# Kernel optimization log

Measured on AMD Instinct MI355X. Metric: run time of the kernel, lower is better.

Reference implementation:

```python
import jax, jax.numpy as jnp
import numpy as np

E = 256  # embed_dim == input_chn (required by ln_ff broadcast)
B = 256
LAMBDA_INIT = float(0.8 - 0.6 * np.exp(-0.3 * 1.0))  # layer_index = 1


def rmsnorm(x, scale, d, eps=1e-8):
    # matches torch RMSNorm: rms = ||x||_2 / sqrt(d); x / (rms + eps) * scale
    norm = jnp.linalg.norm(x, axis=-1, keepdims=True)
    rms = norm * (d ** -0.5)
    return scale * (x / (rms + eps))


def setup_inputs() -> dict:
    key = jax.random.key(0)
    ks = jax.random.split(key, 12)
    x = jax.random.normal(ks[0], (B, E, E), jnp.float32)
    s = 0.02
    return {
        "x": x,
        "Wq": jax.random.normal(ks[1], (E, 2 * E), jnp.float32) * s,
        "bq": jnp.zeros((2 * E,), jnp.float32),
        "Wk": jax.random.normal(ks[2], (E, 2 * E), jnp.float32) * s,
        "bk": jnp.zeros((2 * E,), jnp.float32),
        "Wv": jax.random.normal(ks[3], (E, E), jnp.float32) * s,
        "bv": jnp.zeros((E,), jnp.float32),
        "lq1": jax.random.normal(ks[4], (E,), jnp.float32) * 0.1,
        "lk1": jax.random.normal(ks[5], (E,), jnp.float32) * 0.1,
        "lq2": jax.random.normal(ks[6], (E,), jnp.float32) * 0.1,
        "lk2": jax.random.normal(ks[7], (E,), jnp.float32) * 0.1,
        "ln_attn_scale": jnp.ones((E,), jnp.float32),
        "norm_scale": jnp.ones((E,), jnp.float32),
        "ln_ff_scale": jnp.ones((E,), jnp.float32),
        "W1": jax.random.normal(ks[8], (E, 4 * E), jnp.float32) * s,
        "b1": jnp.zeros((4 * E,), jnp.float32),
        "W2": jax.random.normal(ks[9], (4 * E, E), jnp.float32) * s,
        "b2": jnp.zeros((E,), jnp.float32),
    }


def reference(x, Wq, bq, Wk, bk, Wv, bv, lq1, lk1, lq2, lk2,
              ln_attn_scale, norm_scale, ln_ff_scale, W1, b1, W2, b2):
    scale = E ** -0.25
    # a = ln_attn(x^T)^T  (normalize over seq dim which equals E)
    a = jnp.swapaxes(rmsnorm(jnp.swapaxes(x, -1, -2), ln_attn_scale, E), -1, -2)
    # decompose: moving average kernel=5, stride=1, edge-replicate padding 2 on seq dim
    ap = jnp.pad(a, ((0, 0), (2, 2), (0, 0)), mode="edge")
    trend = (ap[:, 0:-4] + ap[:, 1:-3] + ap[:, 2:-2] + ap[:, 3:-1] + ap[:, 4:]) / 5.0
    seasonal = a - trend
    # Q from trend, K from seasonal, V from a; all projected along the seq(=E) dim
    q = jnp.swapaxes(trend, -1, -2) @ Wq + bq          # [B, C, 2E]
    q1, q2 = jnp.split(q, 2, axis=-1)
    k = jnp.swapaxes(seasonal, -1, -2) @ Wk + bk       # [B, C, 2E]
    k1, k2 = jnp.split(k, 2, axis=-1)
    v = jnp.swapaxes(a, -1, -2) @ Wv + bv              # [B, C, E]
    a1 = jnp.einsum("bce,bde->bcd", q1, k1) * scale    # [B, C, C]
    a2 = jnp.einsum("bce,bde->bcd", q2, k2) * scale
    lam = jnp.exp(jnp.sum(lq1 * lk1)) - jnp.exp(jnp.sum(lq2 * lk2)) + LAMBDA_INIT
    d = jax.nn.softmax(a1, axis=-1) - lam * jax.nn.softmax(a2, axis=-1)
    attn = rmsnorm(d @ v, norm_scale, E) * (1.0 - LAMBDA_INIT)  # [B, C, E]
    x = x + jnp.swapaxes(attn, -1, -2)
    # FFN branch: ln_ff over last dim (chn == E), then project along seq dim
    h = jnp.swapaxes(rmsnorm(x, ln_ff_scale, E), -1, -2)        # [B, C, E]
    h = jax.nn.silu(h @ W1 + b1) @ W2 + b2                      # [B, C, E]
    x = x + jnp.swapaxes(h, -1, -2)
    return x
```

## Files before the change

kernel.cpp:

```cpp
#include <hip/hip_runtime.h>
#include <math.h>

static constexpr int E = 256;
static constexpr int BTOT = 256;

typedef __bf16 bf16;
typedef __bf16 bf16x8 __attribute__((ext_vector_type(8)));
typedef __bf16 bf16x4 __attribute__((ext_vector_type(4)));
typedef float f32x4 __attribute__((ext_vector_type(4)));

__device__ __forceinline__ void gload16(const void* g, void* l) {
  __builtin_amdgcn_global_load_lds(
      (const __attribute__((address_space(1))) void*)g,
      (__attribute__((address_space(3))) void*)l, 16, 0, 0);
}

__device__ __forceinline__ void xcd_decode(int b, int NX, int nPanels, int& x, int& g) {
  if ((nPanels & 7) == 0) {
    int gLo = b & 7;
    int t2 = b >> 3;
    x = t2 % NX;
    g = (t2 / NX) * 8 + gLo;
  } else {
    x = b % NX;
    g = b / NX;
  }
}

__global__ __launch_bounds__(256) void k_wT(const float* __restrict__ src,
                                            bf16* __restrict__ dst, int R, int C) {
  __shared__ float lds[32][33];
  int tiles_c = C >> 5;
  int tc = blockIdx.x % tiles_c;
  int tr = blockIdx.x / tiles_c;
  int r0 = tr << 5, c0 = tc << 5;
  int t = threadIdx.x, cc = t & 31, rr0 = t >> 5;
#pragma unroll
  for (int p = 0; p < 4; ++p) {
    int rr = rr0 + p * 8;
    lds[rr][cc] = src[(size_t)(r0 + rr) * C + (c0 + cc)];
  }
  __syncthreads();
#pragma unroll
  for (int p = 0; p < 4; ++p) {
    int rr = rr0 + p * 8;
    dst[(size_t)(c0 + rr) * R + (r0 + cc)] = (bf16)lds[cc][rr];
  }
}

__global__ void k_lam(const float* lq1, const float* lk1, const float* lq2,
                      const float* lk2, float lambda_init, float* lamOut) {
  int t = threadIdx.x;
  float v1 = lq1[t] * lk1[t];
  float v2 = lq2[t] * lk2[t];
  __shared__ float s1[4], s2[4];
#pragma unroll
  for (int o = 32; o; o >>= 1) { v1 += __shfl_xor(v1, o); v2 += __shfl_xor(v2, o); }
  if ((t & 63) == 0) { s1[t >> 6] = v1; s2[t >> 6] = v2; }
  __syncthreads();
  if (t == 0) {
    float a = s1[0] + s1[1] + s1[2] + s1[3];
    float b = s2[0] + s2[1] + s2[2] + s2[3];
    *lamOut = expf(a) - expf(b) + lambda_init;
  }
}

__global__ __launch_bounds__(1024) void k_rmsA(const float* __restrict__ x, int batchBase,
                                               float* __restrict__ rinvA) {
  __shared__ float red[4][257];
  int lz = blockIdx.x;
  int g = batchBase + lz;
  int t = threadIdx.x, j = t & 255, qd = t >> 8;
  const float* xb = x + (size_t)g * E * E;
  float s = 0.f;
#pragma unroll 4
  for (int ii = 0; ii < 64; ++ii) {
    float v = xb[(size_t)(qd * 64 + ii) * E + j];
    s += v * v;
  }
  red[qd][j] = s;
  __syncthreads();
  if (qd == 0) {
    float tot = red[0][j] + red[1][j] + red[2][j] + red[3][j];
    rinvA[lz * E + j] = __fdividef(1.0f, sqrtf(tot) * 0.0625f + 1e-8f);
  }
}

__global__ __launch_bounds__(256) void k_prep(const float* __restrict__ x, int batchBase,
                                              const float* __restrict__ rinvA,
                                              const float* __restrict__ lnattn,
                                              bf16* __restrict__ a_t,
                                              bf16* __restrict__ tr_t, bf16* __restrict__ se_t) {
  __shared__ float lA[36][261];
  int lz = blockIdx.y, g = batchBase + lz;
  int i0 = blockIdx.x << 5;
  int t = threadIdx.x;
  const float* xb = x + (size_t)g * E * E;
  float rj = rinvA[lz * E + t];
#pragma unroll
  for (int rr = 0; rr < 36; ++rr) {
    int gi = i0 - 2 + rr;
    gi = gi < 0 ? 0 : (gi > 255 ? 255 : gi);
    float v = xb[(size_t)gi * E + t];
    lA[rr][t] = lnattn[gi] * v * rj;
  }
  __syncthreads();
  size_t bo = (size_t)lz * E * E;
  int ic = t & 31, jg = t >> 5;
#pragma unroll 4
  for (int jj = 0; jj < 32; ++jj) {
    int j = jg + jj * 8;
    float a0 = lA[ic][j], a1 = lA[ic + 1][j], a2 = lA[ic + 2][j];
    float a3 = lA[ic + 3][j], a4 = lA[ic + 4][j];
    float tr = (a0 + a1 + a2 + a3 + a4) * 0.2f;
    size_t o = bo + (size_t)j * E + i0 + ic;
    a_t[o] = (bf16)a2;
    tr_t[o] = (bf16)tr;
    se_t[o] = (bf16)(a2 - tr);
  }
}

__device__ __forceinline__ float fsig(float x) {
  return __fdividef(1.0f, 1.0f + __expf(-x));
}

template <int EPI>
__global__ __launch_bounds__(256) void gemm_bt(
    const bf16* __restrict__ A, int lda, size_t aStride,
    const bf16* __restrict__ B, int ldb, size_t bStride,
    bf16* __restrict__ Out, int ldo, size_t oStride, int K,
    const float* __restrict__ biasN, const float* __restrict__ biasM,
    int NX, int NY, int nPanels) {
  __shared__ __align__(128) bf16 As[128][64];
  __shared__ __align__(128) bf16 Bs[128][64];
  int xdec, gdec;
  xcd_decode(blockIdx.x, NX, nPanels, xdec, gdec);
  int lz = gdec / NY;
  int mb = (gdec % NY) << 7, nb = xdec << 7;
  const bf16* Ab = A + (size_t)lz * aStride;
  const bf16* Bb = B + (size_t)lz * bStride;
  int t = threadIdx.x, lane = t & 63, wv = t >> 6;
  int wr = wv >> 1, wc = wv & 1;
  int lrow = lane >> 3;
  int kel = ((lane & 7) ^ lrow) << 3;
  f32x4 acc[4][4];
  const f32x4 z4 = {0.f, 0.f, 0.f, 0.f};
#pragma unroll
  for (int a = 0; a < 4; ++a)
#pragma unroll
    for (int b = 0; b < 4; ++b) acc[a][b] = z4;
  for (int k0 = 0; k0 < K; k0 += 64) {
    __syncthreads();
#pragma unroll
    for (int i = 0; i < 4; ++i) {
      int rb = i * 32 + wv * 8;
      gload16(&Ab[(size_t)(mb + rb + lrow) * lda + k0 + kel], &As[rb][0]);
      gload16(&Bb[(size_t)(nb + rb + lrow) * ldb + k0 + kel], &Bs[rb][0]);
    }
    __syncthreads();
#pragma unroll
    for (int kk = 0; kk < 2; ++kk) {
      int kb = (kk * 64 + ((lane >> 4) << 4)) ^ ((lane & 7) << 4);
      bf16x8 af[4], bfr[4];
#pragma unroll
      for (int mi = 0; mi < 4; ++mi)
        af[mi] = *(const bf16x8*)((const char*)As + (wr * 64 + mi * 16 + (lane & 15)) * 128 + kb);
#pragma unroll
      for (int ni = 0; ni < 4; ++ni)
        bfr[ni] = *(const bf16x8*)((const char*)Bs + (wc * 64 + ni * 16 + (lane & 15)) * 128 + kb);
#pragma unroll
      for (int mi = 0; mi < 4; ++mi)
#pragma unroll
        for (int ni = 0; ni < 4; ++ni)
          acc[mi][ni] = __builtin_amdgcn_mfma_f32_16x16x32_bf16(af[mi], bfr[ni],
                                                                acc[mi][ni], 0, 0, 0);
    }
  }
  int colB = nb + wc * 64 + (lane & 15);
  int rowB = mb + wr * 64 + ((lane >> 4) << 2);
#pragma unroll
  for (int mi = 0; mi < 4; ++mi) {
#pragma unroll
    for (int ni = 0; ni < 4; ++ni) {
      int col = colB + ni * 16;
      float bN = 0.f;
      if constexpr (EPI == 1 || EPI == 3) bN = biasN[col];
#pragma unroll
      for (int r = 0; r < 4; ++r) {
        int row = rowB + mi * 16 + r;
        float v = acc[mi][ni][r];
        if constexpr (EPI == 1) {
          Out[(size_t)lz * oStride + (size_t)row * ldo + col] = (bf16)(v + bN);
        } else if constexpr (EPI == 2) {
          Out[(size_t)lz * oStride + (size_t)row * ldo + col] = (bf16)(v + biasM[row]);
        } else {
          float u = v + bN;
          Out[(size_t)lz * oStride + (size_t)row * ldo + col] = (bf16)(u * fsig(u));
        }
      }
    }
  }
}

__global__ __launch_bounds__(512) void k_score(const bf16* __restrict__ q,
                                               const bf16* __restrict__ km,
                                               const float* __restrict__ lamPtr,
                                               bf16* __restrict__ D, int nPanels) {
  __shared__ __align__(128) bf16 As[128][64];
  __shared__ __align__(128) bf16 Bs[256][64];
  __shared__ float red[4][128];
  int xdec, lz;
  xcd_decode(blockIdx.x, 2, nPanels, xdec, lz);
  int mb = xdec << 7;
  const bf16* qb = q + (size_t)lz * E * 512;
  const bf16* kb = km + (size_t)lz * E * 512;
  int t = threadIdx.x, lane = t & 63, wv = t >> 6;
  int wr = wv >> 2, wc = wv & 3;
  int lrow = lane >> 3;
  int kel = ((lane & 7) ^ lrow) << 3;
  f32x4 acc1[4][4], acc2[4][4];
  const f32x4 z4 = {0.f, 0.f, 0.f, 0.f};
#pragma unroll
  for (int a = 0; a < 4; ++a)
#pragma unroll
    for (int b = 0; b < 4; ++b) { acc1[a][b] = z4; acc2[a][b] = z4; }
#pragma unroll
  for (int mat = 0; mat < 2; ++mat) {
    f32x4(*acc)[4] = mat == 0 ? acc1 : acc2;
    const bf16* qm = qb + mat * 256;
    const bf16* kmm = kb + mat * 256;
    for (int k0 = 0; k0 < 256; k0 += 64) {
      __syncthreads();
#pragma unroll
      for (int i = 0; i < 2; ++i) {
        int rb = i * 64 + wv * 8;
        gload16(&qm[(size_t)(mb + rb + lrow) * 512 + k0 + kel], &As[rb][0]);
      }
#pragma unroll
      for (int i = 0; i < 4; ++i) {
        int rb = i * 64 + wv * 8;
        gload16(&kmm[(size_t)(rb + lrow) * 512 + k0 + kel], &Bs[rb][0]);
      }
      __syncthreads();
#pragma unroll
      for (int kk = 0; kk < 2; ++kk) {
        int kb2 = (kk * 64 + ((lane >> 4) << 4)) ^ ((lane & 7) << 4);
        bf16x8 af[4], bfr[4];
#pragma unroll
        for (int mi = 0; mi < 4; ++mi)
          af[mi] = *(const bf16x8*)((const char*)As + (wr * 64 + mi * 16 + (lane & 15)) * 128 + kb2);
#pragma unroll
        for (int ni = 0; ni < 4; ++ni)
          bfr[ni] = *(const bf16x8*)((const char*)Bs + (wc * 64 + ni * 16 + (lane & 15)) * 128 + kb2);
#pragma unroll
        for (int mi = 0; mi < 4; ++mi)
#pragma unroll
          for (int ni = 0; ni < 4; ++ni)
            acc[mi][ni] = __builtin_amdgcn_mfma_f32_16x16x32_bf16(af[mi], bfr[ni],
                                                                  acc[mi][ni], 0, 0, 0);
      }
    }
  }
  float lam = *lamPtr;
  int rbase = wr * 64 + ((lane >> 4) << 2);
  float inv1[4][4], inv2[4][4];
  __syncthreads();
#pragma unroll
  for (int mat = 0; mat < 2; ++mat) {
    f32x4(*acc)[4] = mat == 0 ? acc1 : acc2;
    float(*inv)[4] = mat == 0 ? inv1 : inv2;
    float tmp[4][4];
#pragma unroll
    for (int mi = 0; mi < 4; ++mi)
#pragma unroll
      for (int r = 0; r < 4; ++r) {
        float m = fmaxf(fmaxf(acc[mi][0][r], acc[mi][1][r]),
                        fmaxf(acc[mi][2][r], acc[mi][3][r]));
        m = fmaxf(m, __shfl_xor(m, 1));
        m = fmaxf(m, __shfl_xor(m, 2));
        m = fmaxf(m, __shfl_xor(m, 4));
        m = fmaxf(m, __shfl_xor(m, 8));
        tmp[mi][r] = m;
      }
    if ((lane & 15) == 0) {
#pragma unroll
      for (int mi = 0; mi < 4; ++mi)
#pragma unroll
        for (int r = 0; r < 4; ++r) red[wc][rbase + mi * 16 + r] = tmp[mi][r];
    }
    __syncthreads();
#pragma unroll
    for (int mi = 0; mi < 4; ++mi)
#pragma unroll
      for (int r = 0; r < 4; ++r) {
        int rw = rbase + mi * 16 + r;
        tmp[mi][r] = fmaxf(fmaxf(red[0][rw], red[1][rw]), fmaxf(red[2][rw], red[3][rw]));
      }
    __syncthreads();
#pragma unroll
    for (int mi = 0; mi < 4; ++mi)
#pragma unroll
      for (int r = 0; r < 4; ++r) {
        float m = tmp[mi][r], s = 0.f;
#pragma unroll
        for (int ni = 0; ni < 4; ++ni) {
          float p = __expf(0.25f * (acc[mi][ni][r] - m));
          acc[mi][ni][r] = p;
          s += p;
        }
        s += __shfl_xor(s, 1);
        s += __shfl_xor(s, 2);
        s += __shfl_xor(s, 4);
        s += __shfl_xor(s, 8);
        tmp[mi][r] = s;
      }
    if ((lane & 15) == 0) {
#pragma unroll
      for (int mi = 0; mi < 4; ++mi)
#pragma unroll
        for (int r = 0; r < 4; ++r) red[wc][rbase + mi * 16 + r] = tmp[mi][r];
    }
    __syncthreads();
#pragma unroll
    for (int mi = 0; mi < 4; ++mi)
#pragma unroll
      for (int r = 0; r < 4; ++r) {
        int rw = rbase + mi * 16 + r;
        inv[mi][r] = __fdividef(1.0f, red[0][rw] + red[1][rw] + red[2][rw] + red[3][rw]);
      }
    __syncthreads();
  }
  size_t Dbase = (size_t)lz * E * E;
#pragma unroll
  for (int mi = 0; mi < 4; ++mi)
#pragma unroll
    for (int ni = 0; ni < 4; ++ni) {
      int col = wc * 64 + ni * 16 + (lane & 15);
#pragma unroll
      for (int r = 0; r < 4; ++r) {
        int row = mb + rbase + mi * 16 + r;
        D[Dbase + (size_t)row * E + col] =
            (bf16)(acc1[mi][ni][r] * inv1[mi][r] - lam * acc2[mi][ni][r] * inv2[mi][r]);
      }
    }
}

__global__ __launch_bounds__(512) void k_pv(const bf16* __restrict__ Dm,
                                            const bf16* __restrict__ vT,
                                            const float* __restrict__ x, int batchBase,
                                            const float* __restrict__ nscale,
                                            float oml, bf16* __restrict__ Y, int nPanels) {
  __shared__ __align__(128) bf16 As[128][64];
  __shared__ __align__(128) bf16 Bs[256][64];
  __shared__ float red[4][128];
  int xdec, lz;
  xcd_decode(blockIdx.x, 2, nPanels, xdec, lz);
  int mb = xdec << 7;
  const bf16* Ab = Dm + (size_t)lz * E * E;
  const bf16* Bb = vT + (size_t)lz * E * E;
  int t = threadIdx.x, lane = t & 63, wv = t >> 6;
  int wr = wv >> 2, wc = wv & 3;
  int lrow = lane >> 3;
  int kel = ((lane & 7) ^ lrow) << 3;
  f32x4 acc[4][4];
  const f32x4 z4 = {0.f, 0.f, 0.f, 0.f};
#pragma unroll
  for (int a = 0; a < 4; ++a)
#pragma unroll
    for (int b = 0; b < 4; ++b) acc[a][b] = z4;
  for (int k0 = 0; k0 < 256; k0 += 64) {
    __syncthreads();
#pragma unroll
    for (int i = 0; i < 2; ++i) {
      int rb = i * 64 + wv * 8;
      gload16(&Ab[(size_t)(mb + rb + lrow) * E + k0 + kel], &As[rb][0]);
    }
#pragma unroll
    for (int i = 0; i < 4; ++i) {
      int rb = i * 64 + wv * 8;
      gload16(&Bb[(size_t)(rb + lrow) * E + k0 + kel], &Bs[rb][0]);
    }
    __syncthreads();
#pragma unroll
    for (int kk = 0; kk < 2; ++kk) {
      int kb2 = (kk * 64 + ((lane >> 4) << 4)) ^ ((lane & 7) << 4);
      bf16x8 af[4], bfr[4];
#pragma unroll
      for (int mi = 0; mi < 4; ++mi)
        af[mi] = *(const bf16x8*)((const char*)As + (wr * 64 + mi * 16 + (lane & 15)) * 128 + kb2);
#pragma unroll
      for (int ni = 0; ni < 4; ++ni)
        bfr[ni] = *(const bf16x8*)((const char*)Bs + (wc * 64 + ni * 16 + (lane & 15)) * 128 + kb2);
#pragma unroll
      for (int mi = 0; mi < 4; ++mi)
#pragma unroll
        for (int ni = 0; ni < 4; ++ni)
          acc[mi][ni] = __builtin_amdgcn_mfma_f32_16x16x32_bf16(af[mi], bfr[ni],
                                                                acc[mi][ni], 0, 0, 0);
    }
  }
  int rbase = wr * 64 + ((lane >> 4) << 2);
  float rowinv[4][4];
#pragma unroll
  for (int mi = 0; mi < 4; ++mi)
#pragma unroll
    for (int r = 0; r < 4; ++r) {
      float s = 0.f;
#pragma unroll
      for (int ni = 0; ni < 4; ++ni) {
        float v = acc[mi][ni][r];
        s += v * v;
      }
      s += __shfl_xor(s, 1);
      s += __shfl_xor(s, 2);
      s += __shfl_xor(s, 4);
      s += __shfl_xor(s, 8);
      rowinv[mi][r] = s;
    }
  if ((lane & 15) == 0) {
#pragma unroll
    for (int mi = 0; mi < 4; ++mi)
#pragma unroll
      for (int r = 0; r < 4; ++r) red[wc][rbase + mi * 16 + r] = rowinv[mi][r];
  }
  __syncthreads();
#pragma unroll
  for (int mi = 0; mi < 4; ++mi)
#pragma unroll
    for (int r = 0; r < 4; ++r) {
      int rw = rbase + mi * 16 + r;
      float tot = red[0][rw] + red[1][rw] + red[2][rw] + red[3][rw];
      rowinv[mi][r] = oml * __fdividef(1.0f, sqrtf(tot) * 0.0625f + 1e-8f);
    }
  size_t bo = (size_t)lz * E * E;
  const float* xb = x + (size_t)(batchBase + lz) * E * E;
#pragma unroll
  for (int mi = 0; mi < 4; ++mi)
#pragma unroll
    for (int ni = 0; ni < 4; ++ni) {
      int col = wc * 64 + ni * 16 + (lane & 15);
      float ns = nscale[col];
      int row0 = mb + rbase + mi * 16;
      f32x4 xv = *(const f32x4*)&xb[(size_t)col * E + row0];
#pragma unroll
      for (int r = 0; r < 4; ++r) {
        size_t o = bo + (size_t)(row0 + r) * E + col;
        Y[o] = (bf16)(xv[r] + ns * acc[mi][ni][r] * rowinv[mi][r]);
      }
    }
}

__global__ __launch_bounds__(256) void k_ffnorm(const bf16* __restrict__ Y,
                                                const float* __restrict__ lnff,
                                                bf16* __restrict__ xn) {
  __shared__ float red[8][33];
  __shared__ float rl[32];
  int lz = blockIdx.y;
  int i0 = blockIdx.x << 5;
  int t = threadIdx.x, ic = t & 31, jg = t >> 5;
  size_t bo = (size_t)lz * E * E;
  float s = 0.f;
#pragma unroll 4
  for (int jj = 0; jj < 32; ++jj) {
    int j = jg + jj * 8;
    float v = (float)Y[bo + (size_t)j * E + i0 + ic];
    s += v * v;
  }
  red[jg][ic] = s;
  __syncthreads();
  if (jg == 0) {
    float tot = 0.f;
#pragma unroll
    for (int g2 = 0; g2 < 8; ++g2) tot += red[g2][ic];
    rl[ic] = __fdividef(1.0f, sqrtf(tot) * 0.0625f + 1e-8f);
  }
  __syncthreads();
  float rinv = rl[ic];
#pragma unroll 4
  for (int jj = 0; jj < 32; ++jj) {
    int j = jg + jj * 8;
    size_t o = bo + (size_t)j * E + i0 + ic;
    xn[o] = (bf16)(lnff[j] * (float)Y[o] * rinv);
  }
}

__global__ __launch_bounds__(256) void k_fin(const bf16* __restrict__ W2T,
                                             const bf16* __restrict__ h1,
                                             const float* __restrict__ b2,
                                             const bf16* __restrict__ Y, int batchBase,
                                             float* __restrict__ out, int nPanels) {
  __shared__ __align__(128) bf16 As[64][64];
  __shared__ __align__(128) bf16 Bs[64][64];
  int ydec, gdec;
  xcd_decode(blockIdx.x, 4, nPanels, ydec, gdec);
  int lz = gdec >> 2;
  int nb = (gdec & 3) << 6;
  int mb = ydec << 6;
  const bf16* Bb = h1 + (size_t)lz * E * 1024;
  int t = threadIdx.x, lane = t & 63, wv = t >> 6;
  int wr = wv >> 1, wc = wv & 1;
  int lrow = lane >> 3;
  int kel = ((lane & 7) ^ lrow) << 3;
  f32x4 acc[2][2];
  const f32x4 z4 = {0.f, 0.f, 0.f, 0.f};
  acc[0][0] = z4; acc[0][1] = z4; acc[1][0] = z4; acc[1][1] = z4;
  for (int k0 = 0; k0 < 1024; k0 += 64) {
    __syncthreads();
#pragma unroll
    for (int i = 0; i < 2; ++i) {
      int rb = i * 32 + wv * 8;
      gload16(&W2T[(size_t)(mb + rb + lrow) * 1024 + k0 + kel], &As[rb][0]);
      gload16(&Bb[(size_t)(nb + rb + lrow) * 1024 + k0 + kel], &Bs[rb][0]);
    }
    __syncthreads();
#pragma unroll
    for (int kk = 0; kk < 2; ++kk) {
      int kb2 = (kk * 64 + ((lane >> 4) << 4)) ^ ((lane & 7) << 4);
      bf16x8 af[2], bfr[2];
#pragma unroll
      for (int mi = 0; mi < 2; ++mi)
        af[mi] = *(const bf16x8*)((const char*)As + (wr * 32 + mi * 16 + (lane & 15)) * 128 + kb2);
#pragma unroll
      for (int ni = 0; ni < 2; ++ni)
        bfr[ni] = *(const bf16x8*)((const char*)Bs + (wc * 32 + ni * 16 + (lane & 15)) * 128 + kb2);
#pragma unroll
      for (int mi = 0; mi < 2; ++mi)
#pragma unroll
        for (int ni = 0; ni < 2; ++ni)
          acc[mi][ni] = __builtin_amdgcn_mfma_f32_16x16x32_bf16(af[mi], bfr[ni],
                                                                acc[mi][ni], 0, 0, 0);
    }
  }
  float* ob = out + (size_t)(batchBase + lz) * E * E;
  const bf16* Yb = Y + (size_t)lz * E * E;
  int rbase = mb + wr * 32 + ((lane >> 4) << 2);
#pragma unroll
  for (int mi = 0; mi < 2; ++mi) {
    int row0 = rbase + mi * 16;
    f32x4 bv = *(const f32x4*)&b2[row0];
#pragma unroll
    for (int ni = 0; ni < 2; ++ni) {
      int col = nb + wc * 32 + ni * 16 + (lane & 15);
      bf16x4 yv = *(const bf16x4*)&Yb[(size_t)col * E + row0];
#pragma unroll
      for (int r = 0; r < 4; ++r)
        ob[(size_t)(row0 + r) * E + col] = acc[mi][ni][r] + bv[r] + (float)yv[r];
    }
  }
}

extern "C" void kernel_launch(void* const* d_in, const int* in_sizes, int n_in,
                              void* d_out, int out_size, void* d_ws, size_t ws_size,
                              hipStream_t stream) {
  const float* x = (const float*)d_in[0];
  const float* Wq = (const float*)d_in[1];
  const float* bq = (const float*)d_in[2];
  const float* Wk = (const float*)d_in[3];
  const float* bk = (const float*)d_in[4];
  const float* Wv = (const float*)d_in[5];
  const float* bv = (const float*)d_in[6];
  const float* lq1 = (const float*)d_in[7];
  const float* lk1 = (const float*)d_in[8];
  const float* lq2 = (const float*)d_in[9];
  const float* lk2 = (const float*)d_in[10];
  const float* lnattn = (const float*)d_in[11];
  const float* nscale = (const float*)d_in[12];
  const float* lnff = (const float*)d_in[13];
  const float* W1 = (const float*)d_in[14];
  const float* b1 = (const float*)d_in[15];
  const float* W2 = (const float*)d_in[16];
  const float* b2 = (const float*)d_in[17];
  float* out = (float*)d_out;

  char* ws = (char*)d_ws;
  size_t off = 0;
  auto alloc = [&](size_t bytes) {
    size_t o = off;
    off += (bytes + 255) & ~(size_t)255;
    return o;
  };
  size_t oWqT = alloc(512 * 256 * 2);
  size_t oWkT = alloc(512 * 256 * 2);
  size_t oWvT = alloc(256 * 256 * 2);
  size_t oW1T = alloc(1024 * 256 * 2);
  size_t oW2T = alloc(256 * 1024 * 2);
  size_t oLam = alloc(256);
  size_t weightEnd = off;

  const size_t szH = (size_t)E * E * 2;
  const size_t szQ = (size_t)E * 512 * 2;
  const size_t szRi = 1024;
  size_t perBatch = 4 * szH + 2 * szQ + szRi;
  size_t avail = ws_size > weightEnd ? ws_size - weightEnd : 0;
  int NB = (int)(avail / perBatch);
  if (NB > BTOT) NB = BTOT;
  if (NB < 1) NB = 1;

  size_t o = weightEnd;
  auto allocN = [&](size_t bytes) {
    size_t r = o;
    o += bytes * (size_t)NB;
    return r;
  };
  bf16* pA = (bf16*)(ws + allocN(szH));
  bf16* pTr = (bf16*)(ws + allocN(szH));
  bf16* pSe = (bf16*)(ws + allocN(szH));
  bf16* pVT = (bf16*)(ws + allocN(szH));
  size_t oQK = allocN(2 * szQ);
  float* pRiA = (float*)(ws + allocN(szRi));

  bf16* pQ = (bf16*)(ws + oQK);
  bf16* pK = (bf16*)(ws + oQK + (size_t)NB * szQ);
  bf16* pD = pTr;
  bf16* pY = pA;
  bf16* pXn = pSe;
  bf16* pH1 = (bf16*)(ws + oQK);

  bf16* pWqT = (bf16*)(ws + oWqT);
  bf16* pWkT = (bf16*)(ws + oWkT);
  bf16* pWvT = (bf16*)(ws + oWvT);
  bf16* pW1T = (bf16*)(ws + oW1T);
  bf16* pW2T = (bf16*)(ws + oW2T);
  float* pLam = (float*)(ws + oLam);

  const float LAMBDA_INIT = 0.8f - 0.6f * expf(-0.3f);
  const float OML = 1.0f - LAMBDA_INIT;

  k_wT<<<dim3((256 / 32) * (512 / 32)), 256, 0, stream>>>(Wq, pWqT, 256, 512);
  k_wT<<<dim3((256 / 32) * (512 / 32)), 256, 0, stream>>>(Wk, pWkT, 256, 512);
  k_wT<<<dim3((256 / 32) * (256 / 32)), 256, 0, stream>>>(Wv, pWvT, 256, 256);
  k_wT<<<dim3((256 / 32) * (1024 / 32)), 256, 0, stream>>>(W1, pW1T, 256, 1024);
  k_wT<<<dim3((1024 / 32) * (256 / 32)), 256, 0, stream>>>(W2, pW2T, 1024, 256);
  k_lam<<<1, 256, 0, stream>>>(lq1, lk1, lq2, lk2, LAMBDA_INIT, pLam);

  for (int base = 0; base < BTOT; base += NB) {
    int cnt = BTOT - base < NB ? BTOT - base : NB;
    k_rmsA<<<dim3(cnt), 1024, 0, stream>>>(x, base, pRiA);
    k_prep<<<dim3(8, cnt), 256, 0, stream>>>(x, base, pRiA, lnattn, pA, pTr, pSe);
    gemm_bt<1><<<dim3(4 * 2 * cnt), 256, 0, stream>>>(pTr, 256, 65536, pWqT, 256, 0,
        pQ, 512, 131072, 256, bq, nullptr, 4, 2, 2 * cnt);
    gemm_bt<1><<<dim3(4 * 2 * cnt), 256, 0, stream>>>(pSe, 256, 65536, pWkT, 256, 0,
        pK, 512, 131072, 256, bk, nullptr, 4, 2, 2 * cnt);
    gemm_bt<2><<<dim3(2 * 2 * cnt), 256, 0, stream>>>(pWvT, 256, 0, pA, 256, 65536,
        pVT, 256, 65536, 256, nullptr, bv, 2, 2, 2 * cnt);
    k_score<<<dim3(2 * cnt), 512, 0, stream>>>(pQ, pK, pLam, pD, cnt);
    k_pv<<<dim3(2 * cnt), 512, 0, stream>>>(pD, pVT, x, base, nscale, OML, pY, cnt);
    k_ffnorm<<<dim3(8, cnt), 256, 0, stream>>>(pY, lnff, pXn);
    gemm_bt<3><<<dim3(8 * 2 * cnt), 256, 0, stream>>>(pXn, 256, 65536, pW1T, 256, 0,
        pH1, 1024, 262144, 256, b1, nullptr, 8, 2, 2 * cnt);
    k_fin<<<dim3(4 * 4 * cnt), 256, 0, stream>>>(pW2T, pH1, b2, pY, base, out, 4 * cnt);
  }
}
```

Baseline: 562.7 us.

## Fuse FFN up-projection, SiLU and down-projection into one LDS-resident kernel

Replaces the separate W1 GEMM with SiLU epilogue and the W2 GEMM (k_fin) with a single 1024-thread kernel. Each block handles 64 channels of one batch, keeps the SiLU hidden activations for a 256-wide chunk in swizzled LDS, and streams W1/W2 tiles through double-buffered LDS. This removes the global write and re-read of the large h1 intermediate. In exchange it uses 128KB of LDS per block with only 4*cnt blocks, which limits occupancy, and every block re-reads the full weights.

```diff
diff --git a/kernel.cpp b/kernel.cpp
--- a/kernel.cpp
+++ b/kernel.cpp
@@ -25,6 +25,10 @@
     x = b % NX;
     g = b / NX;
   }
+}
+
+__device__ __forceinline__ float fsig(float x) {
+  return __fdividef(1.0f, 1.0f + __expf(-x));
 }
 
 __global__ __launch_bounds__(256) void k_wT(const float* __restrict__ src,
@@ -118,10 +122,6 @@
     tr_t[o] = (bf16)tr;
     se_t[o] = (bf16)(a2 - tr);
   }
-}
-
-__device__ __forceinline__ float fsig(float x) {
-  return __fdividef(1.0f, 1.0f + __expf(-x));
 }
 
 template <int EPI>
@@ -184,18 +184,15 @@
     for (int ni = 0; ni < 4; ++ni) {
       int col = colB + ni * 16;
       float bN = 0.f;
-      if constexpr (EPI == 1 || EPI == 3) bN = biasN[col];
+      if constexpr (EPI == 1) bN = biasN[col];
 #pragma unroll
       for (int r = 0; r < 4; ++r) {
         int row = rowB + mi * 16 + r;
         float v = acc[mi][ni][r];
         if constexpr (EPI == 1) {
           Out[(size_t)lz * oStride + (size_t)row * ldo + col] = (bf16)(v + bN);
-        } else if constexpr (EPI == 2) {
+        } else {
           Out[(size_t)lz * oStride + (size_t)row * ldo + col] = (bf16)(v + biasM[row]);
-        } else {
-          float u = v + bN;
-          Out[(size_t)lz * oStride + (size_t)row * ldo + col] = (bf16)(u * fsig(u));
         }
       }
     }
@@ -484,67 +481,165 @@
   }
 }
 
-__global__ __launch_bounds__(256) void k_fin(const bf16* __restrict__ W2T,
-                                             const bf16* __restrict__ h1,
-                                             const float* __restrict__ b2,
-                                             const bf16* __restrict__ Y, int batchBase,
-                                             float* __restrict__ out, int nPanels) {
-  __shared__ __align__(128) bf16 As[64][64];
-  __shared__ __align__(128) bf16 Bs[64][64];
-  int ydec, gdec;
-  xcd_decode(blockIdx.x, 4, nPanels, ydec, gdec);
-  int lz = gdec >> 2;
-  int nb = (gdec & 3) << 6;
-  int mb = ydec << 6;
-  const bf16* Bb = h1 + (size_t)lz * E * 1024;
+__global__ __launch_bounds__(1024) void k_ffn(const bf16* __restrict__ xn,
+                                              const bf16* __restrict__ W1T,
+                                              const bf16* __restrict__ W2T,
+                                              const float* __restrict__ b1,
+                                              const float* __restrict__ b2,
+                                              const bf16* __restrict__ Y,
+                                              int batchBase, float* __restrict__ out) {
+  __shared__ __align__(128) char arena[131072];
+  char* Hb = arena;
+  char* xnL = arena + 32768;
+  char* S0 = arena + 65536;
+  char* S1 = arena + 98304;
+  int bid = blockIdx.x;
+  int lz = bid >> 2;
+  int c0 = (bid & 3) << 6;
+  const bf16* xb = xn + (size_t)lz * E * E + (size_t)c0 * E;
   int t = threadIdx.x, lane = t & 63, wv = t >> 6;
-  int wr = wv >> 1, wc = wv & 1;
   int lrow = lane >> 3;
   int kel = ((lane & 7) ^ lrow) << 3;
-  f32x4 acc[2][2];
+  int l15 = lane & 15, l4 = lane >> 4, l7 = lane & 7;
+  int wr1 = wv >> 3, wc1 = wv & 7;
+  int wr2 = wv >> 1, wc2 = wv & 1;
+
+  float b1v[4][2];
+#pragma unroll
+  for (int ch = 0; ch < 4; ++ch)
+#pragma unroll
+    for (int ni = 0; ni < 2; ++ni)
+      b1v[ch][ni] = b1[ch * 256 + wc1 * 32 + ni * 16 + l15];
+
+#pragma unroll
+  for (int j = 0; j < 2; ++j) {
+    int lin = wv * 2 + j;
+    int ksub = lin >> 3, rg = (lin & 7) * 8;
+    gload16(&xb[(size_t)(rg + lrow) * E + ksub * 64 + kel], xnL + ksub * 8192 + rg * 128);
+  }
+#pragma unroll
+  for (int i = 0; i < 2; ++i) {
+    int rb = i * 128 + wv * 8;
+    gload16(&W1T[(size_t)(rb + lrow) * 256 + kel], S0 + rb * 128);
+  }
+
+  f32x4 acc2[2][2];
   const f32x4 z4 = {0.f, 0.f, 0.f, 0.f};
-  acc[0][0] = z4; acc[0][1] = z4; acc[1][0] = z4; acc[1][1] = z4;
-  for (int k0 = 0; k0 < 1024; k0 += 64) {
-    __syncthreads();
-#pragma unroll
-    for (int i = 0; i < 2; ++i) {
-      int rb = i * 32 + wv * 8;
-      gload16(&W2T[(size_t)(mb + rb + lrow) * 1024 + k0 + kel], &As[rb][0]);
-      gload16(&Bb[(size_t)(nb + rb + lrow) * 1024 + k0 + kel], &Bs[rb][0]);
-    }
-    __syncthreads();
-#pragma unroll
-    for (int kk = 0; kk < 2; ++kk) {
-      int kb2 = (kk * 64 + ((lane >> 4) << 4)) ^ ((lane & 7) << 4);
-      bf16x8 af[2], bfr[2];
-#pragma unroll
-      for (int mi = 0; mi < 2; ++mi)
-        af[mi] = *(const bf16x8*)((const char*)As + (wr * 32 + mi * 16 + (lane & 15)) * 128 + kb2);
-#pragma unroll
-      for (int ni = 0; ni < 2; ++ni)
-        bfr[ni] = *(const bf16x8*)((const char*)Bs + (wc * 32 + ni * 16 + (lane & 15)) * 128 + kb2);
-#pragma unroll
-      for (int mi = 0; mi < 2; ++mi)
+  acc2[0][0] = z4; acc2[0][1] = z4; acc2[1][0] = z4; acc2[1][1] = z4;
+  int cur = 0;
+
+  for (int ch = 0; ch < 4; ++ch) {
+    f32x4 acc1[2][2];
+    acc1[0][0] = z4; acc1[0][1] = z4; acc1[1][0] = z4; acc1[1][1] = z4;
+    for (int k = 0; k < 4; ++k) {
+      char* Sn = cur ? S0 : S1;
+      if (k < 3) {
+#pragma unroll
+        for (int i = 0; i < 2; ++i) {
+          int rb = i * 128 + wv * 8;
+          gload16(&W1T[(size_t)(ch * 256 + rb + lrow) * 256 + (k + 1) * 64 + kel], Sn + rb * 128);
+        }
+      } else {
+#pragma unroll
+        for (int i = 0; i < 2; ++i) {
+          int rb = i * 128 + wv * 8;
+          gload16(&W2T[(size_t)(rb + lrow) * 1024 + ch * 256 + kel], Sn + rb * 128);
+        }
+      }
+      asm volatile("s_waitcnt vmcnt(2)" ::: "memory");
+      __builtin_amdgcn_s_barrier();
+      char* Sc = cur ? S1 : S0;
+#pragma unroll
+      for (int kk = 0; kk < 2; ++kk) {
+        int kb = (kk * 64 + (l4 << 4)) ^ (l7 << 4);
+        bf16x8 af[2], bfr[2];
+#pragma unroll
+        for (int mi = 0; mi < 2; ++mi)
+          af[mi] = *(const bf16x8*)(xnL + k * 8192 + (wr1 * 32 + mi * 16 + l15) * 128 + kb);
 #pragma unroll
         for (int ni = 0; ni < 2; ++ni)
-          acc[mi][ni] = __builtin_amdgcn_mfma_f32_16x16x32_bf16(af[mi], bfr[ni],
-                                                                acc[mi][ni], 0, 0, 0);
-    }
-  }
+          bfr[ni] = *(const bf16x8*)(Sc + (wc1 * 32 + ni * 16 + l15) * 128 + kb);
+#pragma unroll
+        for (int mi = 0; mi < 2; ++mi)
+#pragma unroll
+          for (int ni = 0; ni < 2; ++ni)
+            acc1[mi][ni] = __builtin_amdgcn_mfma_f32_16x16x32_bf16(af[mi], bfr[ni],
+                                                                   acc1[mi][ni], 0, 0, 0);
+      }
+      __builtin_amdgcn_s_barrier();
+      cur ^= 1;
+    }
+#pragma unroll
+    for (int mi = 0; mi < 2; ++mi)
+#pragma unroll
+      for (int ni = 0; ni < 2; ++ni) {
+        int e1 = wc1 * 32 + ni * 16 + l15;
+        float bN = b1v[ch][ni];
+#pragma unroll
+        for (int r = 0; r < 4; ++r) {
+          int c = wr1 * 32 + mi * 16 + l4 * 4 + r;
+          float u = acc1[mi][ni][r] + bN;
+          float h = u * fsig(u);
+          int bo2 = c * 512 + ((((e1 >> 3) ^ (c & 7)) << 4) | ((e1 & 7) * 2));
+          *(bf16*)(Hb + bo2) = (bf16)h;
+        }
+      }
+    asm volatile("s_waitcnt lgkmcnt(0)" ::: "memory");
+    for (int k = 0; k < 4; ++k) {
+      char* Sn = cur ? S0 : S1;
+      bool isLast = (ch == 3) && (k == 3);
+      if (k < 3) {
+#pragma unroll
+        for (int i = 0; i < 2; ++i) {
+          int rb = i * 128 + wv * 8;
+          gload16(&W2T[(size_t)(rb + lrow) * 1024 + ch * 256 + (k + 1) * 64 + kel], Sn + rb * 128);
+        }
+      } else if (ch < 3) {
+#pragma unroll
+        for (int i = 0; i < 2; ++i) {
+          int rb = i * 128 + wv * 8;
+          gload16(&W1T[(size_t)((ch + 1) * 256 + rb + lrow) * 256 + kel], Sn + rb * 128);
+        }
+      }
+      if (isLast) asm volatile("s_waitcnt vmcnt(0)" ::: "memory");
+      else        asm volatile("s_waitcnt vmcnt(2)" ::: "memory");
+      __builtin_amdgcn_s_barrier();
+      char* Sc = cur ? S1 : S0;
+#pragma unroll
+      for (int kk = 0; kk < 2; ++kk) {
+        int kb = (kk * 64 + (l4 << 4)) ^ (l7 << 4);
+        int kbH = (k * 128 + kk * 64 + (l4 << 4)) ^ (l7 << 4);
+        bf16x8 af[2], bfr[2];
+#pragma unroll
+        for (int mi = 0; mi < 2; ++mi)
+          af[mi] = *(const bf16x8*)(Sc + (wr2 * 32 + mi * 16 + l15) * 128 + kb);
+#pragma unroll
+        for (int ni = 0; ni < 2; ++ni)
+          bfr[ni] = *(const bf16x8*)(Hb + (wc2 * 32 + ni * 16 + l15) * 512 + kbH);
+#pragma unroll
+        for (int mi = 0; mi < 2; ++mi)
+#pragma unroll
+          for (int ni = 0; ni < 2; ++ni)
+            acc2[mi][ni] = __builtin_amdgcn_mfma_f32_16x16x32_bf16(af[mi], bfr[ni],
+                                                                   acc2[mi][ni], 0, 0, 0);
+      }
+      __builtin_amdgcn_s_barrier();
+      cur ^= 1;
+    }
+  }
+  const bf16* Yb = Y + (size_t)lz * E * E;
   float* ob = out + (size_t)(batchBase + lz) * E * E;
-  const bf16* Yb = Y + (size_t)lz * E * E;
-  int rbase = mb + wr * 32 + ((lane >> 4) << 2);
 #pragma unroll
   for (int mi = 0; mi < 2; ++mi) {
-    int row0 = rbase + mi * 16;
-    f32x4 bv = *(const f32x4*)&b2[row0];
+    int e2b = wr2 * 32 + mi * 16 + l4 * 4;
+    f32x4 bv = *(const f32x4*)&b2[e2b];
 #pragma unroll
     for (int ni = 0; ni < 2; ++ni) {
-      int col = nb + wc * 32 + ni * 16 + (lane & 15);
-      bf16x4 yv = *(const bf16x4*)&Yb[(size_t)col * E + row0];
+      int c = c0 + wc2 * 32 + ni * 16 + l15;
+      bf16x4 yv = *(const bf16x4*)&Yb[(size_t)c * E + e2b];
 #pragma unroll
       for (int r = 0; r < 4; ++r)
-        ob[(size_t)(row0 + r) * E + col] = acc[mi][ni][r] + bv[r] + (float)yv[r];
+        ob[(size_t)(e2b + r) * E + c] = acc2[mi][ni][r] + bv[r] + (float)yv[r];
     }
   }
 }
@@ -614,7 +709,6 @@
   bf16* pD = pTr;
   bf16* pY = pA;
   bf16* pXn = pSe;
-  bf16* pH1 = (bf16*)(ws + oQK);
 
   bf16* pWqT = (bf16*)(ws + oWqT);
   bf16* pWkT = (bf16*)(ws + oWkT);
@@ -646,8 +740,6 @@
     k_score<<<dim3(2 * cnt), 512, 0, stream>>>(pQ, pK, pLam, pD, cnt);
     k_pv<<<dim3(2 * cnt), 512, 0, stream>>>(pD, pVT, x, base, nscale, OML, pY, cnt);
     k_ffnorm<<<dim3(8, cnt), 256, 0, stream>>>(pY, lnff, pXn);
-    gemm_bt<3><<<dim3(8 * 2 * cnt), 256, 0, stream>>>(pXn, 256, 65536, pW1T, 256, 0,
-        pH1, 1024, 262144, 256, b1, nullptr, 8, 2, 2 * cnt);
-    k_fin<<<dim3(4 * 4 * cnt), 256, 0, stream>>>(pW2T, pH1, b2, pY, base, out, 4 * cnt);
-  }
-}
+    k_ffn<<<dim3(4 * cnt), 1024, 0, stream>>>(pXn, pW1T, pW2T, b1, b2, pY, base, out);
+  }
+}
```

Result: faster. 526.0 us (-6.5%).
